# Kernel optimization log

Hardware: AMD Instinct MI355X
Metric: run time of the kernel (lower is better)

Reference implementation:

```python
import jax, jax.numpy as jnp
import numpy as np

E = 1408      # hidden_size
H = 16        # num heads
D = E // H    # head_dim = 88
S = 1025      # (448/14)^2 + 1 cls token
B = 8


def setup_inputs() -> dict:
    key = jax.random.key(0)
    ks = jax.random.split(key, 11)
    scale = 1.0 / np.sqrt(E)
    inp = {
        "hidden_states": jax.random.normal(ks[0], (B, S, E), dtype=jnp.float32),
    }
    # rotary freqs as cos/sin of random angles, shape (S, D//2)
    theta = jax.random.uniform(ks[1], (S, D // 2), dtype=jnp.float32) * (2.0 * np.pi)
    inp["freqs_cos"] = jnp.cos(theta)
    inp["freqs_sin"] = jnp.sin(theta)
    # projection weights stored torch-style: (out_features, in_features)
    inp["q_w"] = jax.random.normal(ks[2], (E, E), dtype=jnp.float32) * scale
    inp["q_b"] = jax.random.normal(ks[3], (E,), dtype=jnp.float32) * scale
    inp["k_w"] = jax.random.normal(ks[4], (E, E), dtype=jnp.float32) * scale
    inp["k_b"] = jax.random.normal(ks[5], (E,), dtype=jnp.float32) * scale
    inp["v_w"] = jax.random.normal(ks[6], (E, E), dtype=jnp.float32) * scale
    inp["v_b"] = jax.random.normal(ks[7], (E,), dtype=jnp.float32) * scale
    inp["o_w"] = jax.random.normal(ks[8], (E, E), dtype=jnp.float32) * scale
    inp["o_b"] = jax.random.normal(ks[9], (E,), dtype=jnp.float32) * scale
    return inp


def _apply_rope(x, cos, sin):
    # x: (B, S, H, D); interpret last dim as D//2 complex pairs (re, im)
    xr = x.astype(jnp.float32).reshape(*x.shape[:-1], D // 2, 2)
    re, im = xr[..., 0], xr[..., 1]
    c = cos[None, :, None, :]  # broadcast over batch and heads
    s = sin[None, :, None, :]
    out_re = re * c - im * s
    out_im = re * s + im * c
    return jnp.stack([out_re, out_im], axis=-1).reshape(x.shape).astype(x.dtype)


def reference(hidden_states, freqs_cos, freqs_sin, q_w, q_b, k_w, k_b, v_w, v_b, o_w, o_b):
    b, s, _ = hidden_states.shape
    q = (hidden_states @ q_w.T + q_b).reshape(b, s, H, D)
    k = (hidden_states @ k_w.T + k_b).reshape(b, s, H, D)
    v = (hidden_states @ v_w.T + v_b).reshape(b, s, H, D)
    q = _apply_rope(q, freqs_cos, freqs_sin)
    k = _apply_rope(k, freqs_cos, freqs_sin)
    # (B, H, S, D)
    q = q.transpose(0, 2, 1, 3)
    k = k.transpose(0, 2, 1, 3)
    v = v.transpose(0, 2, 1, 3)
    scores = jnp.einsum('bhqd,bhkd->bhqk', q, k) / np.sqrt(D)
    attn = jax.nn.softmax(scores.astype(jnp.float32), axis=-1).astype(q.dtype)
    out = jnp.einsum('bhqk,bhkd->bqhd', attn, v).reshape(b, s, H * D)
    out = out @ o_w.T + o_b
    return out, attn
```

## Files before the change

kernel.cpp:

```cpp
#include <hip/hip_runtime.h>

typedef unsigned short u16;
typedef __attribute__((ext_vector_type(8))) short short8;
typedef __attribute__((ext_vector_type(4))) float f32x4;
typedef __attribute__((ext_vector_type(16))) float f32x16;

#define E_DIM 1408
#define H_HEADS 16
#define S_SEQ 1025
#define B_BATCH 8
#define S_PAD 1088
#define D_PAD 128
#define M_ROWS 8200
#define M_PAD 8320
#define N_QKV 4224

struct __attribute__((packed, aligned(4))) f4u { float x, y, z, w; };

__device__ __forceinline__ u16 f2bf(float f){
  union { float f; unsigned u; } x; x.f = f;
  unsigned r = x.u + 0x7fffu + ((x.u >> 16) & 1u);
  return (u16)(r >> 16);
}

__device__ __forceinline__ void gload16(const void* g, void* l){
  __builtin_amdgcn_global_load_lds(
      (const __attribute__((address_space(1))) void*)g,
      (__attribute__((address_space(3))) void*)l, 16, 0, 0);
}

__device__ __forceinline__ f32x4 mfma16(short8 a, short8 b, f32x4 c){
  return __builtin_amdgcn_mfma_f32_16x16x32_bf16(a, b, c, 0, 0, 0);
}
__device__ __forceinline__ f32x16 mfma32(short8 a, short8 b, f32x16 c){
  return __builtin_amdgcn_mfma_f32_32x32x16_bf16(a, b, c, 0, 0, 0);
}

__device__ __forceinline__ unsigned cvtpk(float a, float b){
  unsigned r;
  asm("v_cvt_pk_bf16_f32 %0, %1, %2" : "=v"(r) : "v"(a), "v"(b));
  return r;
}
__device__ __forceinline__ void plswap(unsigned &a, unsigned &b){
  asm("v_permlane32_swap_b32 %0, %1" : "+v"(a), "+v"(b));
}

#define BARX() { asm volatile("" ::: "memory"); __builtin_amdgcn_s_barrier(); asm volatile("" ::: "memory"); }
#define WAITV(n) asm volatile("s_waitcnt vmcnt(" #n ")" ::: "memory")

__global__ __launch_bounds__(256) void cvt_kernel(const float* __restrict__ src,
                                                  u16* __restrict__ dst, int n8){
  int i = blockIdx.x * 256 + threadIdx.x;
  if (i >= n8) return;
  const float4* s4 = (const float4*)src;
  float4 a = s4[2*i], b = s4[2*i+1];
  union { u16 u[8]; short8 v; } o;
  o.u[0]=f2bf(a.x); o.u[1]=f2bf(a.y); o.u[2]=f2bf(a.z); o.u[3]=f2bf(a.w);
  o.u[4]=f2bf(b.x); o.u[5]=f2bf(b.y); o.u[6]=f2bf(b.z); o.u[7]=f2bf(b.w);
  ((short8*)dst)[i] = o.v;
}

__global__ __launch_bounds__(256) void cvt3_kernel(const float* __restrict__ s0,
                                                   const float* __restrict__ s1,
                                                   const float* __restrict__ s2,
                                                   u16* __restrict__ dst, int n8){
  int i = blockIdx.x * 256 + threadIdx.x;
  if (i >= n8) return;
  const float* src = (blockIdx.y == 0) ? s0 : (blockIdx.y == 1) ? s1 : s2;
  u16* d = dst + (size_t)blockIdx.y * n8 * 8;
  const float4* s4 = (const float4*)src;
  float4 a = s4[2*i], b = s4[2*i+1];
  union { u16 u[8]; short8 v; } o;
  o.u[0]=f2bf(a.x); o.u[1]=f2bf(a.y); o.u[2]=f2bf(a.z); o.u[3]=f2bf(a.w);
  o.u[4]=f2bf(b.x); o.u[5]=f2bf(b.y); o.u[6]=f2bf(b.z); o.u[7]=f2bf(b.w);
  ((short8*)d)[i] = o.v;
}

__global__ __launch_bounds__(256) void zero_pads_kernel(u16* __restrict__ Q,
                                                        u16* __restrict__ K,
                                                        u16* __restrict__ Vt){
  int i = blockIdx.x * 256 + threadIdx.x;
  const int n1 = 128 * S_PAD * 8;
  const int n2 = 128 * 63 * 96;
  const int n3 = 128 * 96 * 63;
  if (i < n1){
    int d = 88 + (i & 7); int t = i >> 3;
    int s = t % S_PAD; int bh = t / S_PAD;
    size_t o = ((size_t)bh * S_PAD + s) * D_PAD + d;
    Q[o] = 0; K[o] = 0;
  } else if (i < n1 + n2){
    int j = i - n1;
    int d = j % 96; int t = j / 96;
    int s = 1025 + t % 63; int bh = t / 63;
    size_t o = ((size_t)bh * S_PAD + s) * D_PAD + d;
    Q[o] = 0; K[o] = 0;
  } else if (i < n1 + n2 + n3){
    int j = i - n1 - n2;
    int d = j % 96; int t = j / 96;
    int sp = 1025 + t % 63; int bh = t / 63;
    Vt[((size_t)bh * D_PAD + d) * S_PAD + sp] = 0;
  }
}

template<int MODE>
__global__ __launch_bounds__(256) void gemm_bt(
    const u16* __restrict__ A, const u16* __restrict__ W,
    const float* __restrict__ b_q, const float* __restrict__ b_k,
    const float* __restrict__ b_v,
    u16* __restrict__ Qb, u16* __restrict__ Kb, u16* __restrict__ Vtb,
    float* __restrict__ outF,
    const float* __restrict__ fcos, const float* __restrict__ fsin)
{
  __shared__ u16 As[128*32];
  __shared__ u16 Bs[128*32];
  const int tid = threadIdx.x;
  const int lane = tid & 63, wid = tid >> 6;
  const int cl = lane & 15, grp = lane >> 4;

  const int nwg = (int)(gridDim.x * gridDim.y);
  const int orig = blockIdx.x + gridDim.x * blockIdx.y;
  const int qq = nwg >> 3, rr = nwg & 7;
  const int xcd = orig & 7, kk = orig >> 3;
  const int wg = (xcd < rr ? xcd * (qq + 1) : rr * (qq + 1) + (xcd - rr) * qq) + kk;
  const int bx = wg % (int)gridDim.x, by = wg / (int)gridDim.x;

  const int n0 = bx * 128, m0 = by * 128;
  const int region = (MODE == 0) ? (bx / 11) : 0;
  const int wm = (wid >> 1) * 64, wn = (wid & 1) * 64;
  f32x4 acc[4][4] = {};

  for (int k0 = 0; k0 < E_DIM; k0 += 32){
    __syncthreads();
#pragma unroll
    for (int rd = 0; rd < 2; ++rd){
      int G = rd * 256 + tid;
      int row = G >> 2, cg = G & 3;
      gload16(A + (size_t)(m0 + row) * E_DIM + k0 + cg * 8, (char*)As + (size_t)G * 16);
      gload16(W + (size_t)(n0 + row) * E_DIM + k0 + cg * 8, (char*)Bs + (size_t)G * 16);
    }
    __syncthreads();
    short8 av[4], bv[4];
#pragma unroll
    for (int i = 0; i < 4; ++i) av[i] = *(const short8*)&As[(wm + i*16 + cl)*32 + grp*8];
#pragma unroll
    for (int j = 0; j < 4; ++j) bv[j] = *(const short8*)&Bs[(wn + j*16 + cl)*32 + grp*8];
    __builtin_amdgcn_s_setprio(1);
#pragma unroll
    for (int i = 0; i < 4; ++i)
#pragma unroll
      for (int j = 0; j < 4; ++j)
        acc[i][j] = mfma16(av[i], bv[j], acc[i][j]);
    __builtin_amdgcn_s_setprio(0);
  }

  const float QSCALE = 0.15379181f;

  if (MODE == 2){
#pragma unroll
    for (int j = 0; j < 4; ++j){
      const int scol = n0 + wn + j*16 + cl;
      const int bb = scol / 1025;
      const int spos = scol - bb * 1025;
      const bool ok = (scol < M_ROWS);
#pragma unroll
      for (int i = 0; i < 4; ++i){
#pragma unroll
        for (int r = 0; r < 4; ++r){
          const int jl = m0 + wm + i*16 + grp*4 + r;
          const int hh = jl / 88;
          const int dd = jl - hh * 88;
          float v = acc[i][j][r] + b_v[jl];
          if (ok)
            Vtb[(((size_t)(bb * 16 + hh)) * D_PAD + dd) * S_PAD + spos] = f2bf(v);
        }
      }
    }
    return;
  }

  const float* bias = (MODE == 1) ? b_q : (region == 0 ? b_q : b_k);

#pragma unroll
  for (int i = 0; i < 4; ++i){
#pragma unroll
    for (int j = 0; j < 4; ++j){
      const int jcol = n0 + wn + j*16 + cl;
      const int jl = jcol - region * E_DIM;
      const float bsv = bias[jl];
      const int hh = jl / 88;
      const int dd = jl - hh * 88;
#pragma unroll
      for (int r = 0; r < 4; ++r){
        const int rrow = m0 + wm + i*16 + grp*4 + r;
        float v = acc[i][j][r] + bsv;
        if (MODE == 0){
          float other = __shfl_xor(v, 1);
          int bb = rrow / 1025;
          int spos = rrow - bb * 1025;
          int pp = dd >> 1;
          float c = fcos[spos * 44 + pp];
          float s = fsin[spos * 44 + pp];
          float o = fmaf(v, c, (jl & 1) ? (other * s) : -(other * s));
          if (region == 0) o *= QSCALE;
          if (rrow < M_ROWS){
            size_t dst = (((size_t)(bb * 16 + hh)) * S_PAD + spos) * D_PAD + dd;
            (region ? Kb : Qb)[dst] = f2bf(o);
          }
        } else {
          if (rrow < M_ROWS) outF[(size_t)rrow * E_DIM + jcol] = v;
        }
      }
    }
  }
}

#define STAGE_K(buf, kt)                                                        \
  {                                                                             \
    _Pragma("unroll")                                                           \
    for (int rd = 0; rd < 4; ++rd){                                             \
      int G = rd * 256 + tid;                                                   \
      int row = G >> 4, c = G & 15;                                             \
      gload16(Kg + (size_t)((kt) * 64 + row) * 128 + ((c ^ (row & 15)) * 8),    \
              (char*)&Ks[buf][0] + (size_t)G * 16);                             \
    }                                                                           \
  }

#define STAGE_V(kt)                                                             \
  {                                                                             \
    _Pragma("unroll")                                                           \
    for (int rd = 0; rd < 3; ++rd){                                             \
      int G = rd * 256 + tid;                                                   \
      int row = G >> 3, c = G & 7;                                              \
      gload16(Vg + (size_t)row * S_PAD + (kt) * 64 + ((c ^ (row & 7)) * 8),     \
              (char*)Vs + (size_t)G * 16);                                      \
    }                                                                           \
  }

__global__ __launch_bounds__(256, 3) void attn_kernel(
    const u16* __restrict__ Qb, const u16* __restrict__ Kb,
    const u16* __restrict__ Vtb, float* __restrict__ attn,
    u16* __restrict__ AO, float* __restrict__ dumpf)
{
  __shared__ u16 Ks[2][64 * 128];
  __shared__ u16 Vs[96 * 64];
  const int tid = threadIdx.x, wid = tid >> 6, lane = tid & 63;
  const int q5 = lane & 31, hi = lane >> 5;
  int lin = blockIdx.x + gridDim.x * blockIdx.y;
  lin = (lin & 7) * 144 + (lin >> 3);
  const int qt = lin % 9, bh = lin / 9;
  const int b = bh >> 4, h = bh & 15;
  const u16* __restrict__ Qg = Qb + (size_t)bh * S_PAD * 128;
  const u16* __restrict__ Kg = Kb + (size_t)bh * S_PAD * 128;
  const u16* __restrict__ Vg = Vtb + (size_t)bh * 128 * S_PAD;
  const int qb0 = qt * 128 + wid * 32;
  const int qrow = qb0 + q5;
  const int qrowc = (qrow < S_PAD) ? qrow : (S_PAD - 1);

  short8 qf[6];
#pragma unroll
  for (int ds = 0; ds < 6; ++ds)
    qf[ds] = *(const short8*)&Qg[(size_t)qrowc * 128 + ds * 16 + hi * 8];

  float l0 = 0.f, l1 = 0.f, l2 = 0.f, l3 = 0.f;
  STAGE_K(0, 0);
  for (int kt = 0; kt < 17; ++kt){
    const int cur = kt & 1;
    if (kt < 16){
      STAGE_K(cur ^ 1, kt + 1);
      WAITV(4);
    } else {
      WAITV(0);
    }
    BARX();
#pragma unroll
    for (int ks = 0; ks < 2; ++ks){
      f32x16 sc = {};
      const int krow = ks * 32 + q5;
      __builtin_amdgcn_s_setprio(1);
#pragma unroll
      for (int ds = 0; ds < 6; ++ds){
        int c = ds * 2 + hi;
        short8 kf = *(const short8*)&Ks[cur][krow * 128 + ((c ^ (krow & 15)) * 8)];
        sc = mfma32(kf, qf[ds], sc);
      }
      __builtin_amdgcn_s_setprio(0);
#pragma unroll
      for (int r = 0; r < 16; r += 4){
        l0 += __builtin_amdgcn_exp2f(sc[r]);
        l1 += __builtin_amdgcn_exp2f(sc[r+1]);
        l2 += __builtin_amdgcn_exp2f(sc[r+2]);
        l3 += __builtin_amdgcn_exp2f(sc[r+3]);
      }
    }
    BARX();
  }
  STAGE_K(0, 0);
  STAGE_V(0);
  float l = (l0 + l1) + (l2 + l3);
  l += __shfl_xor(l, 32);
  l -= 63.0f;
  const float lg2l = __builtin_amdgcn_logf(l);

  f32x16 oacc[3] = {};
  for (int kt = 0; kt < 17; ++kt){
    const int cur = kt & 1;
    if (kt < 16) STAGE_K(cur ^ 1, kt + 1);
    if (kt == 0)      { WAITV(7);  }
    else if (kt < 16) { WAITV(39); }
    else              { WAITV(35); }
    BARX();
    short8 pa0[2], pa1[2];
#pragma unroll
    for (int ks = 0; ks < 2; ++ks){
      f32x16 sc = {};
      const int krow = ks * 32 + q5;
      __builtin_amdgcn_s_setprio(1);
#pragma unroll
      for (int ds = 0; ds < 6; ++ds){
        int c = ds * 2 + hi;
        short8 kf = *(const short8*)&Ks[cur][krow * 128 + ((c ^ (krow & 15)) * 8)];
        sc = mfma32(kf, qf[ds], sc);
      }
      __builtin_amdgcn_s_setprio(0);
#pragma unroll
      for (int r = 0; r < 16; ++r) sc[r] = __builtin_amdgcn_exp2f(sc[r] - lg2l);

      if (kt < 16){
        float* arow = (qrow < 1025)
          ? attn + ((size_t)bh * 1025 + qrow) * 1025 + kt * 64 + ks * 32 + 4 * hi
          : dumpf + tid * 16;
#pragma unroll
        for (int g = 0; g < 4; ++g){
          f4u w4 = { sc[4*g], sc[4*g+1], sc[4*g+2], sc[4*g+3] };
          *(f4u*)(arow + 8 * g) = w4;
        }
      } else {
#pragma unroll
        for (int r = 0; r < 16; ++r){
          int kabs = 1024 + ks * 32 + (r & 3) + 8 * (r >> 2) + 4 * hi;
          float* ad = (qrow < 1025 && kabs < 1025)
            ? attn + ((size_t)bh * 1025 + qrow) * 1025 + kabs
            : dumpf + tid * 16 + r;
          *ad = sc[r];
        }
      }

      unsigned w0 = cvtpk(sc[0],  sc[1]),  w1 = cvtpk(sc[2],  sc[3]);
      unsigned w2 = cvtpk(sc[4],  sc[5]),  w3 = cvtpk(sc[6],  sc[7]);
      unsigned w4 = cvtpk(sc[8],  sc[9]),  w5 = cvtpk(sc[10], sc[11]);
      unsigned w6 = cvtpk(sc[12], sc[13]), w7 = cvtpk(sc[14], sc[15]);
      plswap(w0, w2); plswap(w1, w3); plswap(w4, w6); plswap(w5, w7);
      union U { unsigned u[4]; short8 s8; } A0, A1;
      A0.u[0] = w0; A0.u[1] = w1; A0.u[2] = w2; A0.u[3] = w3;
      A1.u[0] = w4; A1.u[1] = w5; A1.u[2] = w6; A1.u[3] = w7;
      pa0[ks] = A0.s8; pa1[ks] = A1.s8;
    }

    if (kt < 16) { WAITV(36); } else { WAITV(32); }
    BARX();
    __builtin_amdgcn_s_setprio(1);
#pragma unroll
    for (int ks = 0; ks < 2; ++ks){
#pragma unroll
      for (int dt = 0; dt < 3; ++dt){
        const int vrow = dt * 32 + q5;
        int c0 = ks * 4 + hi;
        short8 vf0 = *(const short8*)&Vs[vrow * 64 + ((c0 ^ (vrow & 7)) * 8)];
        oacc[dt] = mfma32(pa0[ks], vf0, oacc[dt]);
        int c1 = ks * 4 + 2 + hi;
        short8 vf1 = *(const short8*)&Vs[vrow * 64 + ((c1 ^ (vrow & 7)) * 8)];
        oacc[dt] = mfma32(pa1[ks], vf1, oacc[dt]);
      }
    }
    __builtin_amdgcn_s_setprio(0);
    BARX();
    if (kt < 16) STAGE_V(kt + 1);
  }

#pragma unroll
  for (int dt = 0; dt < 3; ++dt){
    const int d = dt * 32 + q5;
    if (d < 88){
#pragma unroll
      for (int r = 0; r < 16; ++r){
        int qq2 = qb0 + (r & 3) + 8 * (r >> 2) + 4 * hi;
        if (qq2 < 1025)
          AO[((size_t)b * 1025 + qq2) * E_DIM + h * 88 + d] = f2bf(oacc[dt][r]);
      }
    }
  }
}

extern "C" void kernel_launch(void* const* d_in, const int* in_sizes, int n_in,
                              void* d_out, int out_size, void* d_ws, size_t ws_size,
                              hipStream_t stream)
{
  const float* hs   = (const float*)d_in[0];
  const float* fcos = (const float*)d_in[1];
  const float* fsin = (const float*)d_in[2];
  const float* q_w  = (const float*)d_in[3];
  const float* q_b  = (const float*)d_in[4];
  const float* k_w  = (const float*)d_in[5];
  const float* k_b  = (const float*)d_in[6];
  const float* v_w  = (const float*)d_in[7];
  const float* v_b  = (const float*)d_in[8];
  const float* o_w  = (const float*)d_in[9];
  const float* o_b  = (const float*)d_in[10];
  float* out0 = (float*)d_out;
  float* attn = out0 + (size_t)B_BATCH * S_SEQ * E_DIM;

  char* ws = (char*)d_ws;
  size_t off = 0;
  auto take = [&](size_t bytes){
    char* p = ws + off; off += (bytes + 255) & ~(size_t)255; return p;
  };
  u16* Xb   = (u16*)take((size_t)M_PAD * E_DIM * 2);
  u16* Wqkv = (u16*)take((size_t)N_QKV * E_DIM * 2);
  u16* Wo   = (u16*)take((size_t)E_DIM * E_DIM * 2);
  u16* Qb   = (u16*)take((size_t)128 * S_PAD * D_PAD * 2);
  u16* Kb   = (u16*)take((size_t)128 * S_PAD * D_PAD * 2);
  u16* Vtb  = (u16*)take((size_t)128 * D_PAD * S_PAD * 2);
  u16* AO   = (u16*)take((size_t)M_PAD * E_DIM * 2);
  float* dumpf = (float*)take(65536);

  cvt_kernel<<<(1443200 + 255) / 256, 256, 0, stream>>>(hs, Xb, 1443200);
  cvt3_kernel<<<dim3(968, 3), 256, 0, stream>>>(q_w, k_w, v_w, Wqkv, 247808);
  cvt_kernel<<<968, 256, 0, stream>>>(o_w, Wo, 247808);
  zero_pads_kernel<<<10400, 256, 0, stream>>>(Qb, Kb, Vtb);

  gemm_bt<0><<<dim3(22, 65), 256, 0, stream>>>(Xb, Wqkv, q_b, k_b, v_b,
                                               Qb, Kb, Vtb, nullptr, fcos, fsin);
  gemm_bt<2><<<dim3(65, 11), 256, 0, stream>>>(Wqkv + 2 * (size_t)E_DIM * E_DIM, Xb,
                                               q_b, k_b, v_b,
                                               Qb, Kb, Vtb, nullptr, fcos, fsin);

  attn_kernel<<<dim3(9, 128), 256, 0, stream>>>(Qb, Kb, Vtb, attn, AO, dumpf);

  gemm_bt<1><<<dim3(11, 65), 256, 0, stream>>>(AO, Wo, o_b, o_b, o_b,
                                               nullptr, nullptr, nullptr, out0, fcos, fsin);
}
```

Before: 561.7 us.

## Recompute transposed score tile so attention-probability stores coalesce across lanes

Instead of writing the fp32 attention matrix from the key-major MFMA layout (each lane writing strided rows), the kernel recomputes the QK^T tile with operands swapped so lanes index consecutive key columns, then writes scalar stores that coalesce across the wavefront. Per-row log-normalisers are gathered via shuffles beforehand. This doubles the QK^T MFMA work and the exp2 count in the second pass in exchange for better-coalesced writes of the large attn output.

```diff
diff --git a/kernel.cpp b/kernel.cpp
--- a/kernel.cpp
+++ b/kernel.cpp
@@ -14,8 +14,6 @@
 #define M_ROWS 8200
 #define M_PAD 8320
 #define N_QKV 4224
-
-struct __attribute__((packed, aligned(4))) f4u { float x, y, z, w; };
 
 __device__ __forceinline__ u16 f2bf(float f){
   union { float f; unsigned u; } x; x.f = f;
@@ -300,6 +298,10 @@
   l += __shfl_xor(l, 32);
   l -= 63.0f;
   const float lg2l = __builtin_amdgcn_logf(l);
+  float lglr[16];
+#pragma unroll
+  for (int r = 0; r < 16; ++r)
+    lglr[r] = __shfl(lg2l, (r & 3) + 8 * (r >> 2) + 4 * hi, 64);
 
   f32x16 oacc[3] = {};
   for (int kt = 0; kt < 17; ++kt){
@@ -312,8 +314,8 @@
     short8 pa0[2], pa1[2];
 #pragma unroll
     for (int ks = 0; ks < 2; ++ks){
+      const int krow = ks * 32 + q5;
       f32x16 sc = {};
-      const int krow = ks * 32 + q5;
       __builtin_amdgcn_s_setprio(1);
 #pragma unroll
       for (int ds = 0; ds < 6; ++ds){
@@ -324,26 +326,6 @@
       __builtin_amdgcn_s_setprio(0);
 #pragma unroll
       for (int r = 0; r < 16; ++r) sc[r] = __builtin_amdgcn_exp2f(sc[r] - lg2l);
-
-      if (kt < 16){
-        float* arow = (qrow < 1025)
-          ? attn + ((size_t)bh * 1025 + qrow) * 1025 + kt * 64 + ks * 32 + 4 * hi
-          : dumpf + tid * 16;
-#pragma unroll
-        for (int g = 0; g < 4; ++g){
-          f4u w4 = { sc[4*g], sc[4*g+1], sc[4*g+2], sc[4*g+3] };
-          *(f4u*)(arow + 8 * g) = w4;
-        }
-      } else {
-#pragma unroll
-        for (int r = 0; r < 16; ++r){
-          int kabs = 1024 + ks * 32 + (r & 3) + 8 * (r >> 2) + 4 * hi;
-          float* ad = (qrow < 1025 && kabs < 1025)
-            ? attn + ((size_t)bh * 1025 + qrow) * 1025 + kabs
-            : dumpf + tid * 16 + r;
-          *ad = sc[r];
-        }
-      }
 
       unsigned w0 = cvtpk(sc[0],  sc[1]),  w1 = cvtpk(sc[2],  sc[3]);
       unsigned w2 = cvtpk(sc[4],  sc[5]),  w3 = cvtpk(sc[6],  sc[7]);
@@ -354,6 +336,28 @@
       A0.u[0] = w0; A0.u[1] = w1; A0.u[2] = w2; A0.u[3] = w3;
       A1.u[0] = w4; A1.u[1] = w5; A1.u[2] = w6; A1.u[3] = w7;
       pa0[ks] = A0.s8; pa1[ks] = A1.s8;
+
+      f32x16 sc2 = {};
+      __builtin_amdgcn_s_setprio(1);
+#pragma unroll
+      for (int ds = 0; ds < 6; ++ds){
+        int c = ds * 2 + hi;
+        short8 kf = *(const short8*)&Ks[cur][krow * 128 + ((c ^ (krow & 15)) * 8)];
+        sc2 = mfma32(qf[ds], kf, sc2);
+      }
+      __builtin_amdgcn_s_setprio(0);
+      const int kcol = kt * 64 + ks * 32 + q5;
+      const bool kok = (kcol < 1025);
+      float* const abase = attn + (size_t)bh * 1025 * 1025 + kcol;
+#pragma unroll
+      for (int r = 0; r < 16; ++r){
+        float p = __builtin_amdgcn_exp2f(sc2[r] - lglr[r]);
+        const int qq2 = qb0 + (r & 3) + 8 * (r >> 2) + 4 * hi;
+        float* ad = (kok && qq2 < 1025)
+          ? abase + (size_t)qq2 * 1025
+          : dumpf + tid;
+        *ad = p;
+      }
     }
 
     if (kt < 16) { WAITV(36); } else { WAITV(32); }
```

Result: slower. 892.1 us (+58.8%).
